# Optimization experiments

Hardware: AMD Instinct MI355X
Metric: run time of the kernel (lower is better)

## Reference

```python
import jax, jax.numpy as jnp
import numpy as np
from jax import lax

B, C, H, W = 32, 192, 56, 56
HEADS = 8
HD = C // HEADS
SCALE = HD ** -0.5
EPS = 1e-5


def _ln(t, g, b):
    m = jnp.mean(t, axis=-1, keepdims=True)
    v = jnp.mean((t - m) ** 2, axis=-1, keepdims=True)
    return (t - m) / jnp.sqrt(v + EPS) * g + b


def setup_inputs() -> dict:
    ks = jax.random.split(jax.random.key(0), 8)
    x = jax.random.normal(ks[0], (B, C, H, W), jnp.float32)
    bn_gamma = jnp.ones((C,), jnp.float32)
    bn_beta = jnp.zeros((C,), jnp.float32)
    bn_mean = jax.random.normal(ks[1], (C,), jnp.float32) * 0.1
    bn_var = jax.random.uniform(ks[2], (C,), jnp.float32) + 0.5
    conv_w = jax.random.normal(ks[3], (C, 1, 7, 7), jnp.float32) * 0.02  # depthwise, groups=C
    conv_b = jnp.zeros((C,), jnp.float32)
    qkv_w = jax.random.normal(ks[4], (3 * C, C), jnp.float32) * 0.02
    qkv_b = jnp.zeros((3 * C,), jnp.float32)
    ln0_g = jnp.ones((C,), jnp.float32); ln0_b = jnp.zeros((C,), jnp.float32)
    ln1_g = jnp.ones((C,), jnp.float32); ln1_b = jnp.zeros((C,), jnp.float32)
    return {"x": x, "bn_gamma": bn_gamma, "bn_beta": bn_beta, "bn_mean": bn_mean,
            "bn_var": bn_var, "conv_w": conv_w, "conv_b": conv_b,
            "qkv_w": qkv_w, "qkv_b": qkv_b,
            "ln0_g": ln0_g, "ln0_b": ln0_b, "ln1_g": ln1_g, "ln1_b": ln1_b}


def reference(x, bn_gamma, bn_beta, bn_mean, bn_var, conv_w, conv_b,
              qkv_w, qkv_b, ln0_g, ln0_b, ln1_g, ln1_b):
    Bx, Cx, Hx, Wx = x.shape
    N = Hx * Wx
    Bw = Bx * N // 4  # number of 2x2 windows

    # --- window partition: [B,C,H,W] -> [B*N/4, 4, C]
    windows = x.reshape(Bx, Cx, Hx // 2, 2, Wx // 2, 2)
    windows = windows.transpose(0, 2, 4, 3, 5, 1).reshape(Bw, 4, Cx)

    # --- guide-token generator: BN(inference) -> GELU -> depthwise 7x7 s2 conv
    xb = (x - bn_mean[:, None, None]) / jnp.sqrt(bn_var[:, None, None] + EPS)
    xb = xb * bn_gamma[:, None, None] + bn_beta[:, None, None]
    xg = jax.nn.gelu(xb, approximate=False)
    g = lax.conv_general_dilated(xg, conv_w, window_strides=(2, 2),
                                 padding=[(3, 3), (3, 3)],
                                 feature_group_count=Cx,
                                 dimension_numbers=("NCHW", "OIHW", "NCHW"))
    g = g + conv_b[None, :, None, None]              # [B,C,H/2,W/2]
    guide = g.reshape(Bx, Cx, N // 4).transpose(0, 2, 1).reshape(Bw, 1, Cx)

    # --- 5-token windows: guide + 4 local tokens
    tok = jnp.concatenate([guide, windows], axis=1)  # [Bw,5,C]
    t = _ln(tok, ln0_g, ln0_b)

    # --- tiny attention over 5 tokens
    qkv = t @ qkv_w.T + qkv_b                        # [Bw,5,3C]
    qkv = qkv.reshape(Bw, 5, 3, HEADS, HD).transpose(2, 0, 3, 1, 4)  # [3,Bw,h,5,hd]
    q, k, v = qkv[0], qkv[1], qkv[2]
    attn = jax.nn.softmax(jnp.einsum("bhqd,bhkd->bhqk", q, k) * SCALE, axis=-1)
    o = jnp.einsum("bhqk,bhkd->bhqd", attn, v)       # [Bw,h,5,hd]
    o = o.transpose(0, 2, 1, 3).reshape(Bw, 5, Cx)

    out = o[:, 0].reshape(Bx, Hx // 2, Wx // 2, Cx)
    return _ln(out, ln1_g, ln1_b)
```

## Files before the change

kernel.cpp:

```cpp
#include <hip/hip_runtime.h>
#include <hip/hip_bf16.h>
#include <cmath>

#define B_    32
#define C_    192
#define H_    56
#define W_    56
#define EPS_  1e-5f
#define SCALE_ 0.20412414523193154f

using bf = __hip_bfloat16;
typedef __attribute__((ext_vector_type(8))) short short8;
typedef __attribute__((ext_vector_type(4))) float f32x4;

__global__ void k_wconv(const float* __restrict__ qkv_w, bf* __restrict__ wbf) {
    int i = blockIdx.x * 256 + threadIdx.x;
    if (i < 576 * 192) wbf[i] = __float2bfloat16(qkv_w[i]);
}

__global__ __launch_bounds__(256) void k_act_ptok(
        const float* __restrict__ x,
        const float* __restrict__ ln0g, const float* __restrict__ ln0b,
        bf* __restrict__ ptok) {
    __shared__ float tile[C_ * 57];
    __shared__ float mv[W_], rv[W_];
    int b = blockIdx.x / H_, h = blockIdx.x % H_;
    const size_t xbase = ((size_t)b * C_ * H_ + h) * W_;

    for (int f = threadIdx.x; f < C_ * W_; f += 256) {
        int c = f / W_, w = f % W_;
        tile[c * 57 + w] = x[xbase + (size_t)c * (H_ * W_) + w];
    }
    __syncthreads();
    if (threadIdx.x < 224) {
        int p = threadIdx.x >> 2, q = threadIdx.x & 3;
        float S = 0.f, Q = 0.f;
        #pragma unroll 8
        for (int j = 0; j < 48; j++) {
            float v = tile[(q * 48 + j) * 57 + p];
            S += v; Q += v * v;
        }
        S += __shfl_xor(S, 1); Q += __shfl_xor(Q, 1);
        S += __shfl_xor(S, 2); Q += __shfl_xor(Q, 2);
        if (q == 0) {
            float mean = S * (1.f / 192.f);
            float var  = Q * (1.f / 192.f) - mean * mean;
            mv[p] = mean; rv[p] = rsqrtf(var + EPS_);
        }
    }
    __syncthreads();
    const size_t pbase = (((size_t)b * H_ + h) * W_) * C_;
    for (int f = threadIdx.x; f < W_ * C_; f += 256) {
        int p = f / C_, c = f % C_;
        float v = (tile[c * 57 + p] - mv[p]) * rv[p] * ln0g[c] + ln0b[c];
        ptok[pbase + (size_t)p * C_ + c] = __float2bfloat16(v);
    }
}

__global__ __launch_bounds__(256) void k_conv(
        const float* __restrict__ x,
        const float* __restrict__ bn_g, const float* __restrict__ bn_b,
        const float* __restrict__ bn_m, const float* __restrict__ bn_v,
        const float* __restrict__ cw, const float* __restrict__ cb,
        float* __restrict__ gbuf) {
    __shared__ float pl[62 * 63];
    int tid = threadIdx.x;
    int bc = blockIdx.x;
    int c = bc % C_;

    for (int i = tid; i < 62 * 63; i += 256) pl[i] = 0.f;
    __syncthreads();

    float bm = bn_m[c];
    float rs = rsqrtf(bn_v[c] + EPS_) * bn_g[c];
    float bb = bn_b[c];
    const float* xp = x + (size_t)bc * (H_ * W_);
    for (int i = tid; i < 784; i += 256) {
        int row = i / 14, j = i % 14;
        float4 v = *(const float4*)(xp + row * W_ + j * 4);
        float* dst = &pl[(row + 3) * 63 + j * 4 + 3];
        #pragma unroll
        for (int e = 0; e < 4; e++) {
            float xv = (e == 0) ? v.x : (e == 1) ? v.y : (e == 2) ? v.z : v.w;
            float xn = (xv - bm) * rs + bb;
            dst[e] = 0.5f * xn * (1.0f + erff(xn * 0.70710678118654752f));
        }
    }
    __syncthreads();

    float wr[49];
    #pragma unroll
    for (int i = 0; i < 49; i++) wr[i] = cw[c * 49 + i];
    float cbv = cb[c];

    for (int o = tid; o < 784; o += 256) {
        int oh = o / 28, ow = o % 28;
        const float* base = &pl[(2 * oh) * 63 + 2 * ow];
        float acc = cbv;
        #pragma unroll
        for (int kh = 0; kh < 7; kh++) {
            #pragma unroll
            for (int kw = 0; kw < 7; kw++)
                acc += wr[kh * 7 + kw] * base[kh * 63 + kw];
        }
        gbuf[(size_t)bc * 784 + o] = acc;
    }
}

__global__ __launch_bounds__(256) void k_gtok(
        const float* __restrict__ gbuf,
        const float* __restrict__ ln0g, const float* __restrict__ ln0b,
        bf* __restrict__ gtok) {
    __shared__ float tile[C_ * 29];
    __shared__ float mv[28], rv[28];
    int b = blockIdx.x / 28, oh = blockIdx.x % 28;
    size_t gbase = ((size_t)b * C_ * 784) + (size_t)oh * 28;
    for (int f = threadIdx.x; f < C_ * 28; f += 256) {
        int c = f / 28, w = f % 28;
        tile[c * 29 + w] = gbuf[gbase + (size_t)c * 784 + w];
    }
    __syncthreads();
    if (threadIdx.x < 112) {
        int p = threadIdx.x >> 2, q = threadIdx.x & 3;
        float S = 0.f, Q = 0.f;
        #pragma unroll 8
        for (int j = 0; j < 48; j++) {
            float v = tile[(q * 48 + j) * 29 + p];
            S += v; Q += v * v;
        }
        S += __shfl_xor(S, 1); Q += __shfl_xor(Q, 1);
        S += __shfl_xor(S, 2); Q += __shfl_xor(Q, 2);
        if (q == 0) {
            float mean = S * (1.f / 192.f);
            float var  = Q * (1.f / 192.f) - mean * mean;
            mv[p] = mean; rv[p] = rsqrtf(var + EPS_);
        }
    }
    __syncthreads();
    size_t tbase = ((size_t)b * 784 + (size_t)oh * 28) * C_;
    for (int f = threadIdx.x; f < 28 * C_; f += 256) {
        int p = f / C_, c = f % C_;
        float v = (tile[c * 29 + p] - mv[p]) * rv[p] * ln0g[c] + ln0b[c];
        gtok[tbase + (size_t)p * C_ + c] = __float2bfloat16(v);
    }
}

__global__ __launch_bounds__(256) void k_attn(
        const bf* __restrict__ gtok, const bf* __restrict__ ptok,
        const bf* __restrict__ wbf, const float* __restrict__ qkv_b,
        const float* __restrict__ ln1g, const float* __restrict__ ln1b,
        float* __restrict__ out) {
    __shared__ unsigned char Asm_[48 * 384];
    __shared__ bf q0s[8][192];
    __shared__ bf kvs[2][5][8][192];
    int tid = threadIdx.x;
    int wb0 = blockIdx.x * 8;

    for (int idx = tid; idx < 48 * 24; idx += 256) {
        int row = idx / 24, j = idx % 24;
        int t = row >> 3, win = row & 7;
        uint4 val = {0u, 0u, 0u, 0u};
        if (t < 5) {
            const unsigned char* src;
            if (t == 0) {
                src = (const unsigned char*)(gtok + (size_t)(wb0 + win) * C_) + j * 16;
            } else {
                int bw = wb0 + win;
                int b = bw / 784; int rr = bw - b * 784;
                int oh = rr / 28, ow = rr - oh * 28;
                int h = 2 * oh + ((t - 1) >> 1), w = 2 * ow + ((t - 1) & 1);
                src = (const unsigned char*)(ptok + (((size_t)b * H_ + h) * W_ + w) * C_) + j * 16;
            }
            val = *(const uint4*)src;
        }
        *(uint4*)(Asm_ + row * 384 + ((j * 16) ^ ((row & 7) << 4))) = val;
    }
    __syncthreads();

    int wid = tid >> 6, lane = tid & 63, lo = lane & 15, hi = lane >> 4;
    int xorv = (lo & 7) << 4;
    for (int nn = 0; nn < 9; nn++) {
        int nt = nn * 4 + wid;
        int col = nt * 16 + lo;
        int mtop = (nt < 12) ? 1 : 3;
        float bias = qkv_b[col];
        f32x4 acc0 = {bias, bias, bias, bias};
        f32x4 acc1 = acc0, acc2 = acc0;
        const unsigned char* bbase = (const unsigned char*)wbf + (size_t)col * 384 + hi * 16;
        #pragma unroll
        for (int ks = 0; ks < 6; ks++) {
            short8 bfrag = *(const short8*)(bbase + ks * 64);
            int kb = ks * 64 + hi * 16;
            short8 a0 = *(const short8*)(Asm_ + lo * 384 + (kb ^ xorv));
            acc0 = __builtin_amdgcn_mfma_f32_16x16x32_bf16(a0, bfrag, acc0, 0, 0, 0);
            if (mtop > 1) {
                short8 a1 = *(const short8*)(Asm_ + (16 + lo) * 384 + (kb ^ xorv));
                acc1 = __builtin_amdgcn_mfma_f32_16x16x32_bf16(a1, bfrag, acc1, 0, 0, 0);
                short8 a2 = *(const short8*)(Asm_ + (32 + lo) * 384 + (kb ^ xorv));
                acc2 = __builtin_amdgcn_mfma_f32_16x16x32_bf16(a2, bfrag, acc2, 0, 0, 0);
            }
        }
        #pragma unroll
        for (int m = 0; m < 3; m++) {
            if (m < mtop) {
                f32x4 a = (m == 0) ? acc0 : ((m == 1) ? acc1 : acc2);
                #pragma unroll
                for (int r = 0; r < 4; r++) {
                    int row = m * 16 + hi * 4 + r;
                    int t = row >> 3, win = row & 7;
                    if (t < 5) {
                        float v = a[r];
                        if (col < 192) {
                            if (t == 0) q0s[win][col] = __float2bfloat16(v);
                        } else if (col < 384) {
                            kvs[0][t][win][col - 192] = __float2bfloat16(v);
                        } else {
                            kvs[1][t][win][col - 384] = __float2bfloat16(v);
                        }
                    }
                }
            }
        }
    }
    __syncthreads();

    if (tid >= 64) return;
    int win = tid >> 3, hh = tid & 7, base = hh * 24;
    float q[24], o[24];
    #pragma unroll
    for (int d = 0; d < 24; d++) { q[d] = __bfloat162float(q0s[win][base + d]); o[d] = 0.f; }
    float s[5];
    #pragma unroll
    for (int t = 0; t < 5; t++) {
        float a = 0.f;
        #pragma unroll
        for (int d = 0; d < 24; d++) a += q[d] * __bfloat162float(kvs[0][t][win][base + d]);
        s[t] = a * SCALE_;
    }
    float mx = fmaxf(fmaxf(fmaxf(s[0], s[1]), fmaxf(s[2], s[3])), s[4]);
    float sum = 0.f;
    #pragma unroll
    for (int t = 0; t < 5; t++) { s[t] = expf(s[t] - mx); sum += s[t]; }
    float inv = 1.f / sum;
    #pragma unroll
    for (int t = 0; t < 5; t++) {
        float pt = s[t] * inv;
        #pragma unroll
        for (int d = 0; d < 24; d++) o[d] += pt * __bfloat162float(kvs[1][t][win][base + d]);
    }
    float S = 0.f, Q = 0.f;
    #pragma unroll
    for (int d = 0; d < 24; d++) { S += o[d]; Q += o[d] * o[d]; }
    S += __shfl_xor(S, 1); Q += __shfl_xor(Q, 1);
    S += __shfl_xor(S, 2); Q += __shfl_xor(Q, 2);
    S += __shfl_xor(S, 4); Q += __shfl_xor(Q, 4);
    float mean = S * (1.f / 192.f);
    float var  = Q * (1.f / 192.f) - mean * mean;
    float rstd = rsqrtf(var + EPS_);
    size_t ob = (size_t)(wb0 + win) * C_ + base;
    #pragma unroll
    for (int d = 0; d < 24; d++)
        out[ob + d] = (o[d] - mean) * rstd * ln1g[base + d] + ln1b[base + d];
}

extern "C" void kernel_launch(void* const* d_in, const int* in_sizes, int n_in,
                              void* d_out, int out_size, void* d_ws, size_t ws_size,
                              hipStream_t stream) {
    const float* x       = (const float*)d_in[0];
    const float* bn_g    = (const float*)d_in[1];
    const float* bn_b    = (const float*)d_in[2];
    const float* bn_m    = (const float*)d_in[3];
    const float* bn_v    = (const float*)d_in[4];
    const float* conv_w  = (const float*)d_in[5];
    const float* conv_b  = (const float*)d_in[6];
    const float* qkv_w   = (const float*)d_in[7];
    const float* qkv_b   = (const float*)d_in[8];
    const float* ln0g    = (const float*)d_in[9];
    const float* ln0b    = (const float*)d_in[10];
    const float* ln1g    = (const float*)d_in[11];
    const float* ln1b    = (const float*)d_in[12];

    char* ws = (char*)d_ws;
    bf*    ptok = (bf*)(ws);
    bf*    gtok = (bf*)(ws + 38535168);
    bf*    wbf  = (bf*)(ws + 48168960);
    float* gbuf = (float*)(ws + 48390144);

    k_wconv   <<<dim3(432),   dim3(256), 0, stream>>>(qkv_w, wbf);
    k_conv    <<<dim3(B_*C_), dim3(256), 0, stream>>>(x, bn_g, bn_b, bn_m, bn_v,
                                                      conv_w, conv_b, gbuf);
    k_act_ptok<<<dim3(B_*H_), dim3(256), 0, stream>>>(x, ln0g, ln0b, ptok);
    k_gtok    <<<dim3(B_*28), dim3(256), 0, stream>>>(gbuf, ln0g, ln0b, gtok);
    k_attn    <<<dim3(3136),  dim3(256), 0, stream>>>(gtok, ptok, wbf, qkv_b,
                                                      ln1g, ln1b, (float*)d_out);
}
```

Before: 304.8 us.

## Split attention into per-token K/V GEMM, guide QKV GEMM and separate attention kernel

Replaces the fused per-window attention kernel with two MFMA GEMMs and a lightweight attention kernel. The local tokens need only K/V (no Q), and the guide tokens need full QKV, so the Q projection for the four local tokens is skipped. The attention kernel computes guide-query attention and the final LayerNorm per head thread. The trade-off is materializing a large bf16 K/V buffer and guide QKV buffer in global memory, about 77 MB of extra write and read traffic, and the split path only runs if the workspace is large enough.

```diff
diff --git a/kernel.cpp b/kernel.cpp
--- a/kernel.cpp
+++ b/kernel.cpp
@@ -143,6 +143,150 @@
         float v = (tile[c * 29 + p] - mv[p]) * rv[p] * ln0g[c] + ln0b[c];
         gtok[tbase + (size_t)p * C_ + c] = __float2bfloat16(v);
     }
+}
+
+template<int COLOFS>
+__global__ __launch_bounds__(256) void k_gemm(
+        const bf* __restrict__ A, const bf* __restrict__ wbf,
+        const float* __restrict__ qkv_b, bf* __restrict__ out) {
+    __shared__ unsigned char Asm_[128 * 384];
+    int tid = threadIdx.x;
+    size_t r0 = (size_t)blockIdx.x * 128;
+
+    for (int i = tid; i < 128 * 24; i += 256) {
+        int row = i / 24, j = i % 24;
+        uint4 v = *(const uint4*)((const unsigned char*)(A + (r0 + row) * C_) + j * 16);
+        *(uint4*)(Asm_ + row * 384 + ((j * 16) ^ ((row & 7) << 4))) = v;
+    }
+    __syncthreads();
+
+    int wid = tid >> 6, lane = tid & 63, lo = lane & 15, hi = lane >> 4;
+    int xorv = (lo & 7) << 4;
+    constexpr int NT = (576 - COLOFS) / 16;
+    constexpr int OUTW = 576 - COLOFS;
+    for (int nt = wid; nt < NT; nt += 4) {
+        int col = COLOFS + nt * 16 + lo;
+        float bias = qkv_b[col];
+        f32x4 acc[8];
+        #pragma unroll
+        for (int m = 0; m < 8; m++) acc[m] = {bias, bias, bias, bias};
+        const unsigned char* bbase = (const unsigned char*)wbf + (size_t)col * 384 + hi * 16;
+        #pragma unroll
+        for (int ks = 0; ks < 6; ks++) {
+            short8 bfrag = *(const short8*)(bbase + ks * 64);
+            int kb = (ks * 64 + hi * 16) ^ xorv;
+            #pragma unroll
+            for (int m = 0; m < 8; m++) {
+                short8 a = *(const short8*)(Asm_ + (m * 16 + lo) * 384 + kb);
+                acc[m] = __builtin_amdgcn_mfma_f32_16x16x32_bf16(a, bfrag, acc[m], 0, 0, 0);
+            }
+        }
+        #pragma unroll
+        for (int m = 0; m < 8; m++) {
+            #pragma unroll
+            for (int r = 0; r < 4; r++) {
+                int row = m * 16 + hi * 4 + r;
+                out[(r0 + row) * OUTW + (col - COLOFS)] = __float2bfloat16(acc[m][r]);
+            }
+        }
+    }
+}
+
+__global__ __launch_bounds__(256) void k_att2(
+        const bf* __restrict__ kvp, const bf* __restrict__ qkvg,
+        const float* __restrict__ ln1g, const float* __restrict__ ln1b,
+        float* __restrict__ out) {
+    int tg = blockIdx.x * 256 + threadIdx.x;
+    int bw = tg >> 3, hh = tg & 7;
+    int b = bw / 784, rr = bw % 784;
+    int oh = rr / 28, ow = rr % 28;
+
+    const bf* qb = qkvg + (size_t)bw * 576 + hh * 24;
+    float q[24];
+    #pragma unroll
+    for (int j = 0; j < 3; j++) {
+        short8 v = *(const short8*)(qb + j * 8);
+        #pragma unroll
+        for (int e = 0; e < 8; e++)
+            q[j * 8 + e] = __uint_as_float(((unsigned)(unsigned short)v[e]) << 16);
+    }
+    size_t pr[4];
+    #pragma unroll
+    for (int t = 0; t < 4; t++) {
+        int h = 2 * oh + (t >> 1), w = 2 * ow + (t & 1);
+        pr[t] = ((size_t)b * H_ + h) * W_ + w;
+    }
+
+    float s[5];
+    {
+        float a = 0.f;
+        #pragma unroll
+        for (int j = 0; j < 3; j++) {
+            short8 v = *(const short8*)(qb + 192 + j * 8);
+            #pragma unroll
+            for (int e = 0; e < 8; e++)
+                a += q[j * 8 + e] * __uint_as_float(((unsigned)(unsigned short)v[e]) << 16);
+        }
+        s[0] = a * SCALE_;
+    }
+    #pragma unroll
+    for (int t = 0; t < 4; t++) {
+        const bf* kb = kvp + pr[t] * 384 + hh * 24;
+        float a = 0.f;
+        #pragma unroll
+        for (int j = 0; j < 3; j++) {
+            short8 v = *(const short8*)(kb + j * 8);
+            #pragma unroll
+            for (int e = 0; e < 8; e++)
+                a += q[j * 8 + e] * __uint_as_float(((unsigned)(unsigned short)v[e]) << 16);
+        }
+        s[t + 1] = a * SCALE_;
+    }
+    float mx = fmaxf(fmaxf(fmaxf(s[0], s[1]), fmaxf(s[2], s[3])), s[4]);
+    float sum = 0.f;
+    #pragma unroll
+    for (int t = 0; t < 5; t++) { s[t] = expf(s[t] - mx); sum += s[t]; }
+    float inv = 1.f / sum;
+    #pragma unroll
+    for (int t = 0; t < 5; t++) s[t] *= inv;
+
+    float o[24];
+    #pragma unroll
+    for (int d = 0; d < 24; d++) o[d] = 0.f;
+    {
+        #pragma unroll
+        for (int j = 0; j < 3; j++) {
+            short8 v = *(const short8*)(qb + 384 + j * 8);
+            #pragma unroll
+            for (int e = 0; e < 8; e++)
+                o[j * 8 + e] += s[0] * __uint_as_float(((unsigned)(unsigned short)v[e]) << 16);
+        }
+    }
+    #pragma unroll
+    for (int t = 0; t < 4; t++) {
+        const bf* vb = kvp + pr[t] * 384 + 192 + hh * 24;
+        #pragma unroll
+        for (int j = 0; j < 3; j++) {
+            short8 v = *(const short8*)(vb + j * 8);
+            #pragma unroll
+            for (int e = 0; e < 8; e++)
+                o[j * 8 + e] += s[t + 1] * __uint_as_float(((unsigned)(unsigned short)v[e]) << 16);
+        }
+    }
+
+    float S = 0.f, Q = 0.f;
+    #pragma unroll
+    for (int d = 0; d < 24; d++) { S += o[d]; Q += o[d] * o[d]; }
+    S += __shfl_xor(S, 1); Q += __shfl_xor(Q, 1);
+    S += __shfl_xor(S, 2); Q += __shfl_xor(Q, 2);
+    S += __shfl_xor(S, 4); Q += __shfl_xor(Q, 4);
+    float mean = S * (1.f / 192.f);
+    float var  = Q * (1.f / 192.f) - mean * mean;
+    float rstd = rsqrtf(var + EPS_);
+    float* ob = out + (size_t)bw * 192 + hh * 24;
+    #pragma unroll
+    for (int d = 0; d < 24; d++)
+        ob[d] = (o[d] - mean) * rstd * ln1g[hh * 24 + d] + ln1b[hh * 24 + d];
 }
 
 __global__ __launch_bounds__(256) void k_attn(
@@ -284,13 +428,24 @@
     bf*    ptok = (bf*)(ws);
     bf*    gtok = (bf*)(ws + 38535168);
     bf*    wbf  = (bf*)(ws + 48168960);
-    float* gbuf = (float*)(ws + 48390144);
+    bf*    kvp  = (bf*)(ws + 48390144);
+    bf*    qkvg = (bf*)(ws + 125460480);
+    const bool split = (ws_size >= 154361856ULL);
+    float* gbuf = split ? (float*)(ws + 125460480)
+                        : (float*)(ws + 48390144);
 
     k_wconv   <<<dim3(432),   dim3(256), 0, stream>>>(qkv_w, wbf);
     k_conv    <<<dim3(B_*C_), dim3(256), 0, stream>>>(x, bn_g, bn_b, bn_m, bn_v,
                                                       conv_w, conv_b, gbuf);
     k_act_ptok<<<dim3(B_*H_), dim3(256), 0, stream>>>(x, ln0g, ln0b, ptok);
     k_gtok    <<<dim3(B_*28), dim3(256), 0, stream>>>(gbuf, ln0g, ln0b, gtok);
-    k_attn    <<<dim3(3136),  dim3(256), 0, stream>>>(gtok, ptok, wbf, qkv_b,
-                                                      ln1g, ln1b, (float*)d_out);
-}
+    if (split) {
+        k_gemm<192><<<dim3(784), dim3(256), 0, stream>>>(ptok, wbf, qkv_b, kvp);
+        k_gemm<0>  <<<dim3(196), dim3(256), 0, stream>>>(gtok, wbf, qkv_b, qkvg);
+        k_att2     <<<dim3(784), dim3(256), 0, stream>>>(kvp, qkvg, ln1g, ln1b,
+                                                         (float*)d_out);
+    } else {
+        k_attn     <<<dim3(3136), dim3(256), 0, stream>>>(gtok, ptok, wbf, qkv_b,
+                                                          ln1g, ln1b, (float*)d_out);
+    }
+}
```

After: 311.5 us. 1.02x slower.
